# Kernel tuning notes

Hardware: AMD Instinct MI355X
Metric: run time of the kernel (lower is better)

The kernel has to match this reference:

```python
import jax, jax.numpy as jnp
import numpy as np

B, T, DFEAT = 2, 2048, 1024
DIM, DEPTH, H, DH = 512, 2, 8, 64
INNER = H * DH  # 512
MLP = 512
RED1, RED2 = DIM // 16, DIM // 32  # 32, 16
EPS = 1e-5


def _ln(x, g, b):
    m = jnp.mean(x, axis=-1, keepdims=True)
    v = jnp.mean((x - m) ** 2, axis=-1, keepdims=True)
    return (x - m) * jax.lax.rsqrt(v + EPS) * g + b


def _bn_eval(x, g, b, rm, rv):
    # x: [B, C, T]; eval-mode BatchNorm1d with running stats
    return (x - rm[:, None]) * jax.lax.rsqrt(rv[:, None] + EPS) * g[:, None] + b[:, None]


def setup_inputs() -> dict:
    key = jax.random.key(0)
    ks = iter(jax.random.split(key, 64))
    rn = lambda shape, s=0.02: (jax.random.normal(next(ks), shape, dtype=jnp.float32) * s)
    inp = {}
    inp['x'] = jax.random.normal(next(ks), (B, T, DFEAT), dtype=jnp.float32)
    # Temporal embedding conv (k=3, pad=1), OIW layout
    inp['emb_w'] = rn((DIM, DFEAT, 3))
    inp['emb_b'] = jnp.zeros((DIM,), jnp.float32)
    # Transformer: stacked per-layer params [DEPTH, ...]
    inp['ln1_g'] = jnp.ones((DEPTH, DIM), jnp.float32)
    inp['ln1_b'] = jnp.zeros((DEPTH, DIM), jnp.float32)
    inp['wqkvt'] = rn((DEPTH, DIM, 4 * INNER))
    inp['wout'] = rn((DEPTH, 2 * INNER, DIM))
    inp['bout'] = jnp.zeros((DEPTH, DIM), jnp.float32)
    inp['ln2_g'] = jnp.ones((DEPTH, DIM), jnp.float32)
    inp['ln2_b'] = jnp.zeros((DEPTH, DIM), jnp.float32)
    inp['w1'] = rn((DEPTH, DIM, MLP))
    inp['b1'] = jnp.zeros((DEPTH, MLP), jnp.float32)
    inp['w2'] = rn((DEPTH, MLP, DIM))
    inp['b2'] = jnp.zeros((DEPTH, DIM), jnp.float32)
    # NormalHead (k=1 convs -> pointwise), eval-mode BN params
    inp['h1_w'] = rn((RED1, DIM)); inp['h1_b'] = jnp.zeros((RED1,), jnp.float32)
    inp['bn1_g'] = jnp.ones((RED1,), jnp.float32); inp['bn1_b'] = jnp.zeros((RED1,), jnp.float32)
    inp['bn1_m'] = jnp.zeros((RED1,), jnp.float32); inp['bn1_v'] = jnp.ones((RED1,), jnp.float32)
    inp['h2_w'] = rn((RED2, RED1)); inp['h2_b'] = jnp.zeros((RED2,), jnp.float32)
    inp['bn2_g'] = jnp.ones((RED2,), jnp.float32); inp['bn2_b'] = jnp.zeros((RED2,), jnp.float32)
    inp['bn2_m'] = jnp.zeros((RED2,), jnp.float32); inp['bn2_v'] = jnp.ones((RED2,), jnp.float32)
    inp['h3_w'] = rn((1, RED2)); inp['h3_b'] = jnp.zeros((1,), jnp.float32)
    return inp


def _attention(x, wqkvt, wout, bout, attn2):
    b, n, d = x.shape
    qkvt = x @ wqkvt  # [b, n, 4*INNER]
    q, k, v, t = jnp.split(qkvt, 4, axis=-1)
    sp = lambda z: z.reshape(b, n, H, DH).transpose(0, 2, 1, 3)  # b h n d
    q, k, v, t = sp(q), sp(k), sp(v), sp(t)
    scale = DH ** -0.5
    dots = jnp.einsum('bhid,bhjd->bhij', q, k) * scale
    attn1 = jax.nn.softmax(dots, axis=-1)
    out1 = jnp.einsum('bhij,bhjd->bhid', attn1, v)
    out2 = jnp.einsum('ij,bhjd->bhid', attn2, t)
    out = jnp.concatenate([out1, out2], axis=-1)  # b h n 2*DH
    out = out.transpose(0, 2, 1, 3).reshape(b, n, 2 * INNER)
    return out @ wout + bout


def _forward(x, emb_w, emb_b, ln1_g, ln1_b, wqkvt, wout, bout, ln2_g, ln2_b,
             w1, b1, w2, b2, h1_w, h1_b, bn1_g, bn1_b, bn1_m, bn1_v,
             h2_w, h2_b, bn2_g, bn2_b, bn2_m, bn2_v, h3_w, h3_b):
    # Temporal embedding: Conv1d(k=3,pad=1) + ReLU over time axis
    xc = x.transpose(0, 2, 1)  # [B, DFEAT, T]
    emb = jax.lax.conv_general_dilated(xc, emb_w, (1,), 'SAME',
                                       dimension_numbers=('NCH', 'OIH', 'NCH'))
    emb = jax.nn.relu(emb + emb_b[None, :, None])
    h = emb.transpose(0, 2, 1)  # [B, T, DIM]
    # fixed temporal-decay attention matrix (batch/head independent)
    idx = jnp.arange(T, dtype=jnp.float32)
    tg = jnp.abs(idx[None, :] - idx[:, None])
    a2 = jnp.exp(-tg / jnp.float32(np.e))
    attn2 = a2 / a2.sum(-1)  # torch broadcast: divide along last axis
    for l in range(DEPTH):
        h = h + _attention(_ln(h, ln1_g[l], ln1_b[l]), wqkvt[l], wout[l], bout[l], attn2)
        z = _ln(h, ln2_g[l], ln2_b[l])
        z = jax.nn.gelu(z @ w1[l] + b1[l], approximate=False) @ w2[l] + b2[l]
        h = h + z
    # NormalHead on [B, DIM, T] with k=1 convs
    y = h.transpose(0, 2, 1)
    f1 = jnp.einsum('oc,bct->bot', h1_w, y) + h1_b[None, :, None]
    f2 = jnp.einsum('oc,bct->bot', h2_w, jax.nn.relu(_bn_eval(f1, bn1_g, bn1_b, bn1_m, bn1_v))) + h2_b[None, :, None]
    f3 = jnp.einsum('oc,bct->bot', h3_w, jax.nn.relu(_bn_eval(f2, bn2_g, bn2_b, bn2_m, bn2_v))) + h3_b[None, :, None]
    scores = jax.nn.sigmoid(f3)[:, 0, :]  # [B, T]
    return scores


def reference(x, emb_w, emb_b, ln1_g, ln1_b, wqkvt, wout, bout, ln2_g, ln2_b,
              w1, b1, w2, b2, h1_w, h1_b, bn1_g, bn1_b, bn1_m, bn1_v,
              h2_w, h2_b, bn2_g, bn2_b, bn2_m, bn2_v, h3_w, h3_b):
    return _forward(x, emb_w, emb_b, ln1_g, ln1_b, wqkvt, wout, bout, ln2_g, ln2_b,
                    w1, b1, w2, b2, h1_w, h1_b, bn1_g, bn1_b, bn1_m, bn1_v,
                    h2_w, h2_b, bn2_g, bn2_b, bn2_m, bn2_v, h3_w, h3_b)
```

## Files before the change

kernel.cpp:

```cpp
#include <hip/hip_runtime.h>
#include <hip/hip_bf16.h>
#include <math.h>

#define TN 2048
#define BN 2
#define DF 1024
#define DM 512
#define NHD 8
#define DHD 64
#define INV_E 0.36787944117144233f
#define R_DECAY 0.69220062755534635f

typedef float f32x4 __attribute__((ext_vector_type(4)));
typedef __bf16 bf16x8 __attribute__((ext_vector_type(8)));
typedef unsigned short ushort8 __attribute__((ext_vector_type(8)));
typedef unsigned short ushort4v __attribute__((ext_vector_type(4)));
typedef unsigned int u32x4 __attribute__((ext_vector_type(4)));
typedef unsigned short u16;
typedef unsigned int u32;

__device__ inline u16 f2bf(float f) {
    __hip_bfloat16 b = __float2bfloat16(f);
    return __builtin_bit_cast(u16, b);
}
__device__ inline float bf2f(u16 u) {
    unsigned int x = ((unsigned int)u) << 16;
    return __builtin_bit_cast(float, x);
}
__device__ inline bf16x8 ldbf8(const u16* p) {
    return __builtin_bit_cast(bf16x8, *(const ushort8*)p);
}

struct WtrAll {
    const float* src[8];
    u16* dst[8];
    int K[8], N[8], start[8], mask[8], shift[8];
};

__global__ __launch_bounds__(256) void wtr_all_kernel(WtrAll a) {
    __shared__ u16 tile[64][67];
    int bid = blockIdx.x;
    int w = 0;
#pragma unroll
    for (int i = 1; i < 8; ++i)
        if (bid >= a.start[i]) w = i;
    const float* src = a.src[w];
    u16* dst = a.dst[w];
    int K = a.K[w], N = a.N[w];
    int t0 = bid - a.start[w];
    int bx = t0 & a.mask[w], by = t0 >> a.shift[w];
    int t = threadIdx.x;
    int tr = t >> 4, tc = (t & 15) * 4;
#pragma unroll
    for (int rr = 0; rr < 4; ++rr) {
        int kl = tr + rr * 16;
        float4 v = *(const float4*)&src[(size_t)(by * 64 + kl) * N + bx * 64 + tc];
        tile[kl][tc + 0] = f2bf(v.x);
        tile[kl][tc + 1] = f2bf(v.y);
        tile[kl][tc + 2] = f2bf(v.z);
        tile[kl][tc + 3] = f2bf(v.w);
    }
    __syncthreads();
#pragma unroll
    for (int rr = 0; rr < 4; ++rr) {
        int nl = tr + rr * 16;
        ushort4v o;
#pragma unroll
        for (int q = 0; q < 4; ++q) o[q] = tile[tc + q][nl];
        *(ushort4v*)&dst[(size_t)(bx * 64 + nl) * K + by * 64 + tc] = o;
    }
}

__global__ __launch_bounds__(256) void emb_tr_kernel(const float* __restrict__ w,
                                                     u16* __restrict__ dst) {
    int idx = blockIdx.x * 256 + threadIdx.x;
    if (idx >= DM * 3 * DF) return;
    int o = idx / (3 * DF);
    int rem = idx - o * 3 * DF;
    int tap = rem / DF, i = rem - tap * DF;
    dst[idx] = f2bf(w[(size_t)o * 3 * DF + i * 3 + tap]);
}

__global__ __launch_bounds__(256) void sinv_kernel(float* __restrict__ sinv) {
    int j = blockIdx.x * 256 + threadIdx.x;
    if (j >= TN) return;
    float r = __expf(-INV_E);
    float inv1mr = 1.f / (1.f - r);
    float a = (1.f - __expf(-(float)(j + 1) * INV_E)) * inv1mr;
    float b = (r - __expf(-(float)(TN - j) * INV_E)) * inv1mr;
    sinv[j] = 1.f / (a + b);
}

template <int MODE, int BM, int BNT, int LOG_NX, int CONVA>
__global__ __launch_bounds__(256) void gemm2(const u16* __restrict__ A,
                                             const u16* __restrict__ Bt,
                                             const float* __restrict__ bias,
                                             const float* resid, void* outp,
                                             int M, int N, int K) {
    constexpr int MR = BM / 32, NR = BNT / 32;
    constexpr int PA = BM / 64, PB = BNT / 64;
    __shared__ __align__(16) u16 As[2][BM][72];
    __shared__ __align__(16) u16 Bs[2][BNT][72];
    int tid = threadIdx.x;
    int lane = tid & 63, wid = tid >> 6;
    int cpx = gridDim.x >> 3;
    int swz = (blockIdx.x & 7) * cpx + (blockIdx.x >> 3);
    int n0 = (swz & ((1 << LOG_NX) - 1)) * BNT;
    int m0 = (swz >> LOG_NX) * BM;
    int wm = (wid >> 1) * (BM / 2), wn = (wid & 1) * (BNT / 2);
    int fr = lane & 15, kq = (lane >> 4) * 8;
    int srow = tid >> 2, scol = (tid & 3) * 16;
    f32x4 acc[MR][NR] = {};
    const float* xin = (const float*)A;
    const u16* Ap = A + (size_t)(m0 + srow) * K + scol;
    const u16* Bp = Bt + (size_t)(n0 + srow) * K + scol;
    ushort8 ra[PA][2], rb[PB][2];
    float4 raf[PA][4];

    auto loadA = [&](int k0) {
        if constexpr (CONVA) {
            int tap = k0 >> 10;
            int acol = (k0 & 1023) + scol;
#pragma unroll
            for (int p = 0; p < PA; ++p) {
                int row = m0 + srow + p * 64;
                int tt = (row & (TN - 1)) + tap - 1;
                if (tt >= 0 && tt < TN) {
                    const float* s = xin + ((size_t)((row >> 11) * TN + tt)) * DF + acol;
#pragma unroll
                    for (int q = 0; q < 4; ++q) raf[p][q] = *(const float4*)(s + q * 4);
                } else {
#pragma unroll
                    for (int q = 0; q < 4; ++q) raf[p][q] = float4{0.f, 0.f, 0.f, 0.f};
                }
            }
        } else {
#pragma unroll
            for (int p = 0; p < PA; ++p) {
                ra[p][0] = *(const ushort8*)(Ap + (size_t)p * 64 * K + k0);
                ra[p][1] = *(const ushort8*)(Ap + (size_t)p * 64 * K + k0 + 8);
            }
        }
    };
    auto writeA = [&](int pb) {
#pragma unroll
        for (int p = 0; p < PA; ++p) {
            if constexpr (CONVA) {
                ushort8 w0, w1;
#pragma unroll
                for (int q = 0; q < 4; ++q) {
                    w0[q] = f2bf(raf[p][0][q]);
                    w0[4 + q] = f2bf(raf[p][1][q]);
                    w1[q] = f2bf(raf[p][2][q]);
                    w1[4 + q] = f2bf(raf[p][3][q]);
                }
                *(ushort8*)&As[pb][srow + p * 64][scol] = w0;
                *(ushort8*)&As[pb][srow + p * 64][scol + 8] = w1;
            } else {
                *(ushort8*)&As[pb][srow + p * 64][scol] = ra[p][0];
                *(ushort8*)&As[pb][srow + p * 64][scol + 8] = ra[p][1];
            }
        }
    };

    loadA(0);
#pragma unroll
    for (int p = 0; p < PB; ++p) {
        rb[p][0] = *(const ushort8*)(Bp + (size_t)p * 64 * K);
        rb[p][1] = *(const ushort8*)(Bp + (size_t)p * 64 * K + 8);
    }
    int nt = K >> 6;
    int pb = 0;
    for (int t = 0; t < nt; ++t) {
        writeA(pb);
#pragma unroll
        for (int p = 0; p < PB; ++p) {
            *(ushort8*)&Bs[pb][srow + p * 64][scol] = rb[p][0];
            *(ushort8*)&Bs[pb][srow + p * 64][scol + 8] = rb[p][1];
        }
        __syncthreads();
        if (t + 1 < nt) {
            int ko = (t + 1) << 6;
            loadA(ko);
#pragma unroll
            for (int p = 0; p < PB; ++p) {
                rb[p][0] = *(const ushort8*)(Bp + (size_t)p * 64 * K + ko);
                rb[p][1] = *(const ushort8*)(Bp + (size_t)p * 64 * K + ko + 8);
            }
        }
#pragma unroll
        for (int kc = 0; kc < 2; ++kc) {
            bf16x8 af[MR], bf[NR];
#pragma unroll
            for (int a = 0; a < MR; ++a) af[a] = ldbf8(&As[pb][wm + a * 16 + fr][kc * 32 + kq]);
#pragma unroll
            for (int b = 0; b < NR; ++b) bf[b] = ldbf8(&Bs[pb][wn + b * 16 + fr][kc * 32 + kq]);
#pragma unroll
            for (int a = 0; a < MR; ++a)
#pragma unroll
                for (int b = 0; b < NR; ++b)
                    acc[a][b] = __builtin_amdgcn_mfma_f32_16x16x32_bf16(af[a], bf[b], acc[a][b], 0, 0, 0);
        }
        pb ^= 1;
    }
    int rq = (lane >> 4) * 4;
#pragma unroll
    for (int a = 0; a < MR; ++a)
#pragma unroll
        for (int b = 0; b < NR; ++b) {
            int col = n0 + wn + b * 16 + fr;
            float bv = (MODE & 1) ? bias[col] : 0.f;
#pragma unroll
            for (int r = 0; r < 4; ++r) {
                int row = m0 + wm + a * 16 + rq + r;
                float v = acc[a][b][r] + bv;
                if (MODE & 2) v = fmaxf(v, 0.f);
                if (MODE & 4) v = 0.5f * v * (1.f + erff(v * 0.7071067811865476f));
                if (MODE & 8) v += resid[(size_t)row * N + col];
                if (MODE & 16) ((float*)outp)[(size_t)row * N + col] = v;
                else           ((u16*)outp)[(size_t)row * N + col] = f2bf(v);
            }
        }
}

__global__ __launch_bounds__(256) void ln_kernel(const float* __restrict__ h,
                                                 const float* __restrict__ g,
                                                 const float* __restrict__ bta,
                                                 u16* __restrict__ outp) {
    int lane = threadIdx.x & 63, wid = threadIdx.x >> 6;
    int row = blockIdx.x * 4 + wid;
    const float4* xp = (const float4*)(h + (size_t)row * DM + lane * 8);
    float4 v0 = xp[0], v1 = xp[1];
    float v[8] = {v0.x, v0.y, v0.z, v0.w, v1.x, v1.y, v1.z, v1.w};
    float s = 0.f;
#pragma unroll
    for (int i = 0; i < 8; ++i) s += v[i];
    for (int sft = 1; sft < 64; sft <<= 1) s += __shfl_xor(s, sft, 64);
    float mean = s * (1.f / DM);
    float q = 0.f;
#pragma unroll
    for (int i = 0; i < 8; ++i) { float d = v[i] - mean; q += d * d; }
    for (int sft = 1; sft < 64; sft <<= 1) q += __shfl_xor(q, sft, 64);
    float rs = rsqrtf(q * (1.f / DM) + 1e-5f);
    ushort8 o;
#pragma unroll
    for (int i = 0; i < 8; ++i) {
        float y = (v[i] - mean) * rs * g[lane * 8 + i] + bta[lane * 8 + i];
        o[i] = f2bf(y);
    }
    *(ushort8*)&outp[(size_t)row * DM + lane * 8] = o;
}

__global__ __launch_bounds__(256, 4) void attn_split(const u16* __restrict__ qkvt,
                                                     u16* __restrict__ po,
                                                     float* __restrict__ pl) {
    __shared__ __align__(16) u16 Ks[64][72];
    __shared__ __align__(16) u16 Vs[64][72];
    int tid = threadIdx.x;
    int lane = tid & 63, wid = tid >> 6;
    int bid = blockIdx.x;
    int cc = bid & 3, qb = (bid >> 2) & 15, hh = (bid >> 6) & 7, b = bid >> 9;
    int fr = lane & 15, kq = (lane >> 4) * 8, rq = (lane >> 4) * 4;

    bf16x8 aq[2][2];
#pragma unroll
    for (int s = 0; s < 2; ++s)
#pragma unroll
        for (int kc = 0; kc < 2; ++kc) {
            int qrow = qb * 128 + wid * 32 + s * 16 + fr;
            bf16x8 t = ldbf8(&qkvt[((size_t)(b * TN + qrow)) * 2048 + hh * 64 + kc * 32 + kq]);
            bf16x8 sc;
#pragma unroll
            for (int i = 0; i < 8; ++i) sc[i] = (__bf16)(0.125f * (float)t[i]);
            aq[s][kc] = sc;
        }

    f32x4 o[2][4] = {};
    float rsum[2] = {0.f, 0.f};

    int srow = tid >> 3, scol = (tid & 7) * 8;
    int vxw = ((scol >> 3) & 7) << 3;
    int i01 = (fr + ((lane & 16) << 1)) << 2;
    int i23 = i01 + 64;
    bool hi2 = (lane & 32) != 0;

    const u16* kvbase = qkvt + ((size_t)(b * TN + cc * 512 + srow)) * 2048 + hh * 64 + scol;

    ushort8 rk[2], rv[2];
    rk[0] = *(const ushort8*)(kvbase + 512);
    rk[1] = *(const ushort8*)(kvbase + 512 + (size_t)32 * 2048);
    rv[0] = *(const ushort8*)(kvbase + 1024);
    rv[1] = *(const ushort8*)(kvbase + 1024 + (size_t)32 * 2048);

    for (int t = 0; t < 8; ++t) {
        __syncthreads();
#pragma unroll
        for (int half = 0; half < 2; ++half) {
            int jr = srow + half * 32;
            *(ushort8*)&Ks[jr][scol] = rk[half];
            int jc = jr ^ vxw;
#pragma unroll
            for (int i = 0; i < 8; ++i) Vs[scol + i][jc] = rv[half][i];
        }
        __syncthreads();
        if (t < 7) {
            const u16* kb2 = kvbase + (size_t)(t + 1) * 64 * 2048;
            rk[0] = *(const ushort8*)(kb2 + 512);
            rk[1] = *(const ushort8*)(kb2 + 512 + (size_t)32 * 2048);
            rv[0] = *(const ushort8*)(kb2 + 1024);
            rv[1] = *(const ushort8*)(kb2 + 1024 + (size_t)32 * 2048);
        }
        u32 pkr[2][4][2];
#pragma unroll
        for (int jb = 0; jb < 4; ++jb) {
            f32x4 sa0 = f32x4{0.f, 0.f, 0.f, 0.f};
            f32x4 sa1 = f32x4{0.f, 0.f, 0.f, 0.f};
#pragma unroll
            for (int kc = 0; kc < 2; ++kc) {
                bf16x8 bk = ldbf8(&Ks[jb * 16 + fr][kc * 32 + kq]);
                sa0 = __builtin_amdgcn_mfma_f32_16x16x32_bf16(bk, aq[0][kc], sa0, 0, 0, 0);
                sa1 = __builtin_amdgcn_mfma_f32_16x16x32_bf16(bk, aq[1][kc], sa1, 0, 0, 0);
            }
            {
                float p0 = __expf(sa0[0]), p1 = __expf(sa0[1]);
                float p2 = __expf(sa0[2]), p3 = __expf(sa0[3]);
                rsum[0] += (p0 + p1) + (p2 + p3);
                pkr[0][jb][0] = ((u32)f2bf(p1) << 16) | (u32)f2bf(p0);
                pkr[0][jb][1] = ((u32)f2bf(p3) << 16) | (u32)f2bf(p2);
            }
            {
                float p0 = __expf(sa1[0]), p1 = __expf(sa1[1]);
                float p2 = __expf(sa1[2]), p3 = __expf(sa1[3]);
                rsum[1] += (p0 + p1) + (p2 + p3);
                pkr[1][jb][0] = ((u32)f2bf(p1) << 16) | (u32)f2bf(p0);
                pkr[1][jb][1] = ((u32)f2bf(p3) << 16) | (u32)f2bf(p2);
            }
        }
        bf16x8 pa[2][2];
#pragma unroll
        for (int s = 0; s < 2; ++s)
#pragma unroll
            for (int kc = 0; kc < 2; ++kc) {
                u32 a0 = (u32)__builtin_amdgcn_ds_bpermute(i01, (int)pkr[s][kc * 2][0]);
                u32 b0 = (u32)__builtin_amdgcn_ds_bpermute(i01, (int)pkr[s][kc * 2 + 1][0]);
                u32 a1 = (u32)__builtin_amdgcn_ds_bpermute(i01, (int)pkr[s][kc * 2][1]);
                u32 b1 = (u32)__builtin_amdgcn_ds_bpermute(i01, (int)pkr[s][kc * 2 + 1][1]);
                u32 a2 = (u32)__builtin_amdgcn_ds_bpermute(i23, (int)pkr[s][kc * 2][0]);
                u32 b2 = (u32)__builtin_amdgcn_ds_bpermute(i23, (int)pkr[s][kc * 2 + 1][0]);
                u32 a3 = (u32)__builtin_amdgcn_ds_bpermute(i23, (int)pkr[s][kc * 2][1]);
                u32 b3 = (u32)__builtin_amdgcn_ds_bpermute(i23, (int)pkr[s][kc * 2 + 1][1]);
                u32x4 w;
                w[0] = hi2 ? b0 : a0;
                w[1] = hi2 ? b1 : a1;
                w[2] = hi2 ? b2 : a2;
                w[3] = hi2 ? b3 : a3;
                pa[s][kc] = __builtin_bit_cast(bf16x8, w);
            }
#pragma unroll
        for (int cb = 0; cb < 4; ++cb)
#pragma unroll
            for (int kc = 0; kc < 2; ++kc) {
                int vrow = cb * 16 + fr;
                bf16x8 bv = ldbf8(&Vs[vrow][(kc * 32 + kq) ^ (((vrow >> 3) & 7) << 3)]);
                o[0][cb] = __builtin_amdgcn_mfma_f32_16x16x32_bf16(pa[0][kc], bv, o[0][cb], 0, 0, 0);
                o[1][cb] = __builtin_amdgcn_mfma_f32_16x16x32_bf16(pa[1][kc], bv, o[1][cb], 0, 0, 0);
            }
    }
#pragma unroll
    for (int s = 0; s < 2; ++s) {
        rsum[s] += __shfl_xor(rsum[s], 16, 64);
        rsum[s] += __shfl_xor(rsum[s], 32, 64);
    }
#pragma unroll
    for (int s = 0; s < 2; ++s)
#pragma unroll
        for (int r = 0; r < 4; ++r) {
            int grow = (b * NHD + hh) * TN + qb * 128 + wid * 32 + s * 16 + rq + r;
            size_t pidx = (size_t)grow * 4 + cc;
#pragma unroll
            for (int cb = 0; cb < 4; ++cb)
                po[pidx * 64 + cb * 16 + fr] = f2bf(o[s][cb][r]);
        }
    if (lane < 16) {
#pragma unroll
        for (int s = 0; s < 2; ++s) {
            int grow = (b * NHD + hh) * TN + qb * 128 + wid * 32 + s * 16 + fr;
            pl[(size_t)grow * 4 + cc] = rsum[s];
        }
    }
}

#define BCH 32
__global__ __launch_bounds__(256) void postattn_kernel(const u16* __restrict__ po,
                                                       const float* __restrict__ pl,
                                                       const u16* __restrict__ qkvt,
                                                       const float* __restrict__ sinv,
                                                       u16* __restrict__ attcat) {
    int bid = blockIdx.x;
    if (bid < BN * NHD * TN / 4) {
        int lane = threadIdx.x & 63, wid = threadIdx.x >> 6;
        int R = bid * 4 + wid;
        float l = 0.f, ov = 0.f;
#pragma unroll
        for (int cc = 0; cc < 4; ++cc) {
            l += pl[(size_t)R * 4 + cc];
            ov += bf2f(po[((size_t)R * 4 + cc) * 64 + lane]);
        }
        int bh = R >> 11, q = R & (TN - 1);
        int b = bh >> 3, hh = bh & 7;
        attcat[((size_t)(b * TN + q)) * 1024 + hh * 128 + lane] = f2bf(ov / l);
    } else {
        int t2 = (bid - BN * NHD * TN / 4) * 256 + threadIdx.x;
        int c = t2 & 511;
        int rest = t2 >> 9;
        int chunk = rest & 63;
        int b = rest >> 6;
        int i0 = chunk * BCH;
        const float r = R_DECAY;
        const u16* tcol = qkvt + 1536 + c;
        float regs[BCH];
        float st = 0.f;
        for (int j = i0 - 32; j < i0; ++j) {
            if (j >= 0) st = r * st + sinv[j] * bf2f(tcol[(size_t)(b * TN + j) * 2048]);
        }
#pragma unroll
        for (int k = 0; k < BCH; ++k) {
            int j = i0 + k;
            st = r * st + sinv[j] * bf2f(tcol[(size_t)(b * TN + j) * 2048]);
            regs[k] = st;
        }
        st = 0.f;
        for (int j = i0 + BCH + 31; j >= i0 + BCH; --j) {
            if (j < TN) st = r * st + sinv[j] * bf2f(tcol[(size_t)(b * TN + j) * 2048]);
        }
#pragma unroll
        for (int k = BCH - 1; k >= 0; --k) {
            int j = i0 + k;
            regs[k] += r * st;
            st = r * st + sinv[j] * bf2f(tcol[(size_t)(b * TN + j) * 2048]);
        }
        int outcol = (c >> 6) * 128 + 64 + (c & 63);
#pragma unroll
        for (int k = 0; k < BCH; ++k)
            attcat[((size_t)(b * TN + i0 + k)) * 1024 + outcol] = f2bf(regs[k]);
    }
}

__global__ __launch_bounds__(256) void head_kernel(
    const float* __restrict__ h, const float* __restrict__ h1w, const float* __restrict__ h1b,
    const float* __restrict__ bn1g, const float* __restrict__ bn1b,
    const float* __restrict__ bn1m, const float* __restrict__ bn1v,
    const float* __restrict__ h2w, const float* __restrict__ h2b,
    const float* __restrict__ bn2g, const float* __restrict__ bn2b,
    const float* __restrict__ bn2m, const float* __restrict__ bn2v,
    const float* __restrict__ h3w, const float* __restrict__ h3b,
    float* __restrict__ outp) {
    int lane = threadIdx.x & 63, wid = threadIdx.x >> 6;
    int idx = blockIdx.x * 4 + wid;
    const float4* xp = (const float4*)(h + (size_t)idx * DM + lane * 8);
    float4 v0 = xp[0], v1 = xp[1];
    float v[8] = {v0.x, v0.y, v0.z, v0.w, v1.x, v1.y, v1.z, v1.w};
    float a1[32];
#pragma unroll
    for (int o = 0; o < 32; ++o) {
        const float4* wp = (const float4*)(h1w + (size_t)o * DM + lane * 8);
        float4 w0 = wp[0], w1v = wp[1];
        a1[o] = w0.x * v[0] + w0.y * v[1] + w0.z * v[2] + w0.w * v[3] +
                w1v.x * v[4] + w1v.y * v[5] + w1v.z * v[6] + w1v.w * v[7];
    }
    for (int sft = 1; sft < 64; sft <<= 1) {
#pragma unroll
        for (int o = 0; o < 32; ++o) a1[o] += __shfl_xor(a1[o], sft, 64);
    }
    float r1[32];
#pragma unroll
    for (int o = 0; o < 32; ++o) {
        float f = a1[o] + h1b[o];
        f = (f - bn1m[o]) * rsqrtf(bn1v[o] + 1e-5f) * bn1g[o] + bn1b[o];
        r1[o] = fmaxf(f, 0.f);
    }
    float r2[16];
#pragma unroll
    for (int p = 0; p < 16; ++p) {
        float s = h2b[p];
#pragma unroll
        for (int o = 0; o < 32; ++o) s = fmaf(h2w[p * 32 + o], r1[o], s);
        s = (s - bn2m[p]) * rsqrtf(bn2v[p] + 1e-5f) * bn2g[p] + bn2b[p];
        r2[p] = fmaxf(s, 0.f);
    }
    float f3 = h3b[0];
#pragma unroll
    for (int p = 0; p < 16; ++p) f3 = fmaf(h3w[p], r2[p], f3);
    if (lane == 0) outp[idx] = 1.f / (1.f + __expf(-f3));
}

extern "C" void kernel_launch(void* const* d_in, const int* in_sizes, int n_in,
                              void* d_out, int out_size, void* d_ws, size_t ws_size,
                              hipStream_t stream) {
    const float* x     = (const float*)d_in[0];
    const float* emb_w = (const float*)d_in[1];
    const float* emb_b = (const float*)d_in[2];
    const float* ln1_g = (const float*)d_in[3];
    const float* ln1_b = (const float*)d_in[4];
    const float* wqkvt = (const float*)d_in[5];
    const float* wout  = (const float*)d_in[6];
    const float* bout  = (const float*)d_in[7];
    const float* ln2_g = (const float*)d_in[8];
    const float* ln2_b = (const float*)d_in[9];
    const float* w1    = (const float*)d_in[10];
    const float* b1    = (const float*)d_in[11];
    const float* w2    = (const float*)d_in[12];
    const float* b2    = (const float*)d_in[13];
    const float* h1w   = (const float*)d_in[14];
    const float* h1b   = (const float*)d_in[15];
    const float* bn1g  = (const float*)d_in[16];
    const float* bn1b  = (const float*)d_in[17];
    const float* bn1m  = (const float*)d_in[18];
    const float* bn1v  = (const float*)d_in[19];
    const float* h2w   = (const float*)d_in[20];
    const float* h2b   = (const float*)d_in[21];
    const float* bn2g  = (const float*)d_in[22];
    const float* bn2b  = (const float*)d_in[23];
    const float* bn2m  = (const float*)d_in[24];
    const float* bn2v  = (const float*)d_in[25];
    const float* h3w   = (const float*)d_in[26];
    const float* h3b   = (const float*)d_in[27];
    float* outp = (float*)d_out;

    char* ws = (char*)d_ws;
    size_t off = 0;
    auto take = [&](size_t bytes) {
        char* p = ws + off;
        off = (off + bytes + 255) & ~(size_t)255;
        return p;
    };
    const size_t MB = 1024 * 1024;
    float* h    = (float*)take((size_t)BN * TN * DM * 4);
    char* Pr    = take(18 * MB);
    u16* attcat = (u16*)take((size_t)BN * TN * 1024 * 2);
    float* sinv = (float*)take(TN * 4);
    u16* embwt  = (u16*)take((size_t)DM * 3 * DF * 2);
    u16* wqt    = (u16*)take((size_t)2 * 2048 * DM * 2);
    u16* woutt  = (u16*)take((size_t)2 * DM * 1024 * 2);
    u16* w1t    = (u16*)take((size_t)2 * DM * DM * 2);
    u16* w2t    = (u16*)take((size_t)2 * DM * DM * 2);
    u16* qkvtb  = (u16*)take((size_t)BN * TN * 2048 * 2);
    u16* xln  = (u16*)Pr;
    u16* z1   = (u16*)(Pr + 4 * MB);
    float* pl = (float*)Pr;
    u16* po   = (u16*)(Pr + 1 * MB);
    (void)ws_size; (void)in_sizes; (void)n_in; (void)out_size;

    emb_tr_kernel<<<dim3(DM * 3 * DF / 256), dim3(256), 0, stream>>>(emb_w, embwt);
    {
        WtrAll a;
        int cur = 0;
        for (int l = 0; l < 2; ++l) {
            int e = l * 4;
            a.src[e + 0] = wqkvt + (size_t)l * 512 * 2048; a.dst[e + 0] = wqt + (size_t)l * 2048 * 512;
            a.K[e + 0] = 512;  a.N[e + 0] = 2048; a.start[e + 0] = cur; a.mask[e + 0] = 31; a.shift[e + 0] = 5; cur += 256;
            a.src[e + 1] = wout + (size_t)l * 1024 * 512;  a.dst[e + 1] = woutt + (size_t)l * 512 * 1024;
            a.K[e + 1] = 1024; a.N[e + 1] = 512;  a.start[e + 1] = cur; a.mask[e + 1] = 7;  a.shift[e + 1] = 3; cur += 128;
            a.src[e + 2] = w1 + (size_t)l * 512 * 512;     a.dst[e + 2] = w1t + (size_t)l * 512 * 512;
            a.K[e + 2] = 512;  a.N[e + 2] = 512;  a.start[e + 2] = cur; a.mask[e + 2] = 7;  a.shift[e + 2] = 3; cur += 64;
            a.src[e + 3] = w2 + (size_t)l * 512 * 512;     a.dst[e + 3] = w2t + (size_t)l * 512 * 512;
            a.K[e + 3] = 512;  a.N[e + 3] = 512;  a.start[e + 3] = cur; a.mask[e + 3] = 7;  a.shift[e + 3] = 3; cur += 64;
        }
        wtr_all_kernel<<<dim3(cur), dim3(256), 0, stream>>>(a);
    }
    sinv_kernel<<<dim3(TN / 256), dim3(256), 0, stream>>>(sinv);

    gemm2<19, 64, 64, 3, 1><<<dim3((DM / 64) * (BN * TN / 64)), dim3(256), 0, stream>>>(
        (const u16*)x, embwt, emb_b, nullptr, h, BN * TN, DM, 3 * DF);

    for (int l = 0; l < 2; ++l) {
        ln_kernel<<<dim3(BN * TN / 4), dim3(256), 0, stream>>>(h, ln1_g + l * DM, ln1_b + l * DM, xln);
        gemm2<0, 128, 128, 4, 0><<<dim3((2048 / 128) * (BN * TN / 128)), dim3(256), 0, stream>>>(
            xln, wqt + (size_t)l * 2048 * 512, nullptr, nullptr, qkvtb, BN * TN, 2048, DM);
        attn_split<<<dim3(BN * NHD * (TN / 128) * 4), dim3(256), 0, stream>>>(qkvtb, po, pl);
        postattn_kernel<<<dim3(BN * NHD * TN / 4 + BN * 512 * (TN / BCH) / 256), dim3(256), 0, stream>>>(
            po, pl, qkvtb, sinv, attcat);
        gemm2<25, 64, 64, 3, 0><<<dim3((DM / 64) * (BN * TN / 64)), dim3(256), 0, stream>>>(
            attcat, woutt + (size_t)l * 512 * 1024, bout + l * DM, h, h, BN * TN, DM, 1024);
        ln_kernel<<<dim3(BN * TN / 4), dim3(256), 0, stream>>>(h, ln2_g + l * DM, ln2_b + l * DM, xln);
        gemm2<5, 64, 64, 3, 0><<<dim3((DM / 64) * (BN * TN / 64)), dim3(256), 0, stream>>>(
            xln, w1t + (size_t)l * 512 * 512, b1 + l * DM, nullptr, z1, BN * TN, DM, DM);
        gemm2<25, 64, 64, 3, 0><<<dim3((DM / 64) * (BN * TN / 64)), dim3(256), 0, stream>>>(
            z1, w2t + (size_t)l * 512 * 512, b2 + l * DM, h, h, BN * TN, DM, DM);
    }
    head_kernel<<<dim3(BN * TN / 4), dim3(256), 0, stream>>>(
        h, h1w, h1b, bn1g, bn1b, bn1m, bn1v, h2w, h2b, bn2g, bn2b, bn2m, bn2v, h3w, h3b, outp);
}
```

Before: 327.7 us.

## Split embedding conv GEMM over taps and combine partial sums

```diff
diff --git a/kernel.cpp b/kernel.cpp
--- a/kernel.cpp
+++ b/kernel.cpp
@@ -96,7 +96,7 @@
                                              const u16* __restrict__ Bt,
                                              const float* __restrict__ bias,
                                              const float* resid, void* outp,
-                                             int M, int N, int K) {
+                                             int M, int N, int K, int Ks) {
     constexpr int MR = BM / 32, NR = BNT / 32;
     constexpr int PA = BM / 64, PB = BNT / 64;
     __shared__ __align__(16) u16 As[2][BM][72];
@@ -107,20 +107,20 @@
     int swz = (blockIdx.x & 7) * cpx + (blockIdx.x >> 3);
     int n0 = (swz & ((1 << LOG_NX) - 1)) * BNT;
     int m0 = (swz >> LOG_NX) * BM;
+    int tap = CONVA ? blockIdx.y : 0;
     int wm = (wid >> 1) * (BM / 2), wn = (wid & 1) * (BNT / 2);
     int fr = lane & 15, kq = (lane >> 4) * 8;
     int srow = tid >> 2, scol = (tid & 3) * 16;
     f32x4 acc[MR][NR] = {};
     const float* xin = (const float*)A;
-    const u16* Ap = A + (size_t)(m0 + srow) * K + scol;
-    const u16* Bp = Bt + (size_t)(n0 + srow) * K + scol;
+    const u16* Ap = A + (size_t)(m0 + srow) * Ks + scol;
+    const u16* Bp = Bt + (CONVA ? tap * DF : 0) + (size_t)(n0 + srow) * Ks + scol;
     ushort8 ra[PA][2], rb[PB][2];
     float4 raf[PA][4];
 
     auto loadA = [&](int k0) {
         if constexpr (CONVA) {
-            int tap = k0 >> 10;
-            int acol = (k0 & 1023) + scol;
+            int acol = k0 + scol;
 #pragma unroll
             for (int p = 0; p < PA; ++p) {
                 int row = m0 + srow + p * 64;
@@ -137,8 +137,8 @@
         } else {
 #pragma unroll
             for (int p = 0; p < PA; ++p) {
-                ra[p][0] = *(const ushort8*)(Ap + (size_t)p * 64 * K + k0);
-                ra[p][1] = *(const ushort8*)(Ap + (size_t)p * 64 * K + k0 + 8);
+                ra[p][0] = *(const ushort8*)(Ap + (size_t)p * 64 * Ks + k0);
+                ra[p][1] = *(const ushort8*)(Ap + (size_t)p * 64 * Ks + k0 + 8);
             }
         }
     };
@@ -166,8 +166,8 @@
     loadA(0);
 #pragma unroll
     for (int p = 0; p < PB; ++p) {
-        rb[p][0] = *(const ushort8*)(Bp + (size_t)p * 64 * K);
-        rb[p][1] = *(const ushort8*)(Bp + (size_t)p * 64 * K + 8);
+        rb[p][0] = *(const ushort8*)(Bp + (size_t)p * 64 * Ks);
+        rb[p][1] = *(const ushort8*)(Bp + (size_t)p * 64 * Ks + 8);
     }
     int nt = K >> 6;
     int pb = 0;
@@ -184,8 +184,8 @@
             loadA(ko);
 #pragma unroll
             for (int p = 0; p < PB; ++p) {
-                rb[p][0] = *(const ushort8*)(Bp + (size_t)p * 64 * K + ko);
-                rb[p][1] = *(const ushort8*)(Bp + (size_t)p * 64 * K + ko + 8);
+                rb[p][0] = *(const ushort8*)(Bp + (size_t)p * 64 * Ks + ko);
+                rb[p][1] = *(const ushort8*)(Bp + (size_t)p * 64 * Ks + ko + 8);
             }
         }
 #pragma unroll
@@ -204,6 +204,8 @@
         pb ^= 1;
     }
     int rq = (lane >> 4) * 4;
+    float* outc = (float*)outp;
+    if constexpr (CONVA) outc += (size_t)tap * M * N;
 #pragma unroll
     for (int a = 0; a < MR; ++a)
 #pragma unroll
@@ -217,10 +219,27 @@
                 if (MODE & 2) v = fmaxf(v, 0.f);
                 if (MODE & 4) v = 0.5f * v * (1.f + erff(v * 0.7071067811865476f));
                 if (MODE & 8) v += resid[(size_t)row * N + col];
-                if (MODE & 16) ((float*)outp)[(size_t)row * N + col] = v;
+                if (MODE & 16) outc[(size_t)row * N + col] = v;
                 else           ((u16*)outp)[(size_t)row * N + col] = f2bf(v);
             }
         }
+}
+
+__global__ __launch_bounds__(256) void conv_combine_kernel(const float* __restrict__ pc,
+                                                           const float* __restrict__ bias,
+                                                           float* __restrict__ h) {
+    int idx = blockIdx.x * 256 + threadIdx.x;
+    const size_t PS = (size_t)BN * TN * DM;
+    float4 p0 = *(const float4*)(pc + (size_t)idx * 4);
+    float4 p1 = *(const float4*)(pc + PS + (size_t)idx * 4);
+    float4 p2 = *(const float4*)(pc + 2 * PS + (size_t)idx * 4);
+    float4 bv = *(const float4*)(bias + (idx & (DM / 4 - 1)) * 4);
+    float4 o;
+    o.x = fmaxf(p0.x + p1.x + p2.x + bv.x, 0.f);
+    o.y = fmaxf(p0.y + p1.y + p2.y + bv.y, 0.f);
+    o.z = fmaxf(p0.z + p1.z + p2.z + bv.z, 0.f);
+    o.w = fmaxf(p0.w + p1.w + p2.w + bv.w, 0.f);
+    *(float4*)(h + (size_t)idx * 4) = o;
 }
 
 __global__ __launch_bounds__(256) void ln_kernel(const float* __restrict__ h,
@@ -536,7 +555,7 @@
     };
     const size_t MB = 1024 * 1024;
     float* h    = (float*)take((size_t)BN * TN * DM * 4);
-    char* Pr    = take(18 * MB);
+    char* Pr    = take(25 * MB);
     u16* attcat = (u16*)take((size_t)BN * TN * 1024 * 2);
     float* sinv = (float*)take(TN * 4);
     u16* embwt  = (u16*)take((size_t)DM * 3 * DF * 2);
@@ -545,6 +564,7 @@
     u16* w1t    = (u16*)take((size_t)2 * DM * DM * 2);
     u16* w2t    = (u16*)take((size_t)2 * DM * DM * 2);
     u16* qkvtb  = (u16*)take((size_t)BN * TN * 2048 * 2);
+    float* pc = (float*)Pr;
     u16* xln  = (u16*)Pr;
     u16* z1   = (u16*)(Pr + 4 * MB);
     float* pl = (float*)Pr;
@@ -570,23 +590,24 @@
     }
     sinv_kernel<<<dim3(TN / 256), dim3(256), 0, stream>>>(sinv);
 
-    gemm2<19, 64, 64, 3, 1><<<dim3((DM / 64) * (BN * TN / 64)), dim3(256), 0, stream>>>(
-        (const u16*)x, embwt, emb_b, nullptr, h, BN * TN, DM, 3 * DF);
+    gemm2<16, 64, 64, 3, 1><<<dim3((DM / 64) * (BN * TN / 64), 3), dim3(256), 0, stream>>>(
+        (const u16*)x, embwt, nullptr, nullptr, pc, BN * TN, DM, 1024, 3 * DF);
+    conv_combine_kernel<<<dim3(BN * TN * DM / 4 / 256), dim3(256), 0, stream>>>(pc, emb_b, h);
 
     for (int l = 0; l < 2; ++l) {
         ln_kernel<<<dim3(BN * TN / 4), dim3(256), 0, stream>>>(h, ln1_g + l * DM, ln1_b + l * DM, xln);
         gemm2<0, 128, 128, 4, 0><<<dim3((2048 / 128) * (BN * TN / 128)), dim3(256), 0, stream>>>(
-            xln, wqt + (size_t)l * 2048 * 512, nullptr, nullptr, qkvtb, BN * TN, 2048, DM);
+            xln, wqt + (size_t)l * 2048 * 512, nullptr, nullptr, qkvtb, BN * TN, 2048, DM, DM);
         attn_split<<<dim3(BN * NHD * (TN / 128) * 4), dim3(256), 0, stream>>>(qkvtb, po, pl);
         postattn_kernel<<<dim3(BN * NHD * TN / 4 + BN * 512 * (TN / BCH) / 256), dim3(256), 0, stream>>>(
             po, pl, qkvtb, sinv, attcat);
         gemm2<25, 64, 64, 3, 0><<<dim3((DM / 64) * (BN * TN / 64)), dim3(256), 0, stream>>>(
-            attcat, woutt + (size_t)l * 512 * 1024, bout + l * DM, h, h, BN * TN, DM, 1024);
+            attcat, woutt + (size_t)l * 512 * 1024, bout + l * DM, h, h, BN * TN, DM, 1024, 1024);
         ln_kernel<<<dim3(BN * TN / 4), dim3(256), 0, stream>>>(h, ln2_g + l * DM, ln2_b + l * DM, xln);
         gemm2<5, 64, 64, 3, 0><<<dim3((DM / 64) * (BN * TN / 64)), dim3(256), 0, stream>>>(
-            xln, w1t + (size_t)l * 512 * 512, b1 + l * DM, nullptr, z1, BN * TN, DM, DM);
+            xln, w1t + (size_t)l * 512 * 512, b1 + l * DM, nullptr, z1, BN * TN, DM, DM, DM);
         gemm2<25, 64, 64, 3, 0><<<dim3((DM / 64) * (BN * TN / 64)), dim3(256), 0, stream>>>(
-            z1, w2t + (size_t)l * 512 * 512, b2 + l * DM, h, h, BN * TN, DM, DM);
+            z1, w2t + (size_t)l * 512 * 512, b2 + l * DM, h, h, BN * TN, DM, DM, DM);
     }
     head_kernel<<<dim3(BN * TN / 4), dim3(256), 0, stream>>>(
         h, h1w, h1b, bn1g, bn1b, bn1m, bn1v, h2w, h2b, bn2g, bn2b, bn2m, bn2v, h3w, h3b, outp);
```

Result: slower. 335.1 us (+2.3%).
